# Kernel optimization log

Measured on AMD Instinct MI355X. Metric: run time of the kernel, lower is better.

Reference implementation:

```python
import jax, jax.numpy as jnp
import numpy as np

N_NODES = 50000
N_EDGES = 1600000
F_IN = 256
HID = 256
HEADS = 8
HD = HID // HEADS  # 32
SLOPE = 0.2
EPS = 1e-5


def setup_inputs() -> dict:
    key = jax.random.key(0)
    ks = jax.random.split(key, 10)
    node_features = jax.random.normal(ks[0], (N_NODES, F_IN), jnp.float32)
    edge_index = jax.random.randint(ks[1], (2, N_EDGES), 0, N_NODES, jnp.int32)
    s = 1.0 / np.sqrt(F_IN)
    W = jax.random.uniform(ks[2], (HEADS, F_IN, HD), jnp.float32, -s, s)
    bw = jax.random.uniform(ks[3], (HEADS, HD), jnp.float32, -s, s)
    sa = 1.0 / np.sqrt(2 * HD)
    A = jax.random.uniform(ks[4], (HEADS, 2 * HD), jnp.float32, -sa, sa)
    ba = jax.random.uniform(ks[5], (HEADS,), jnp.float32, -sa, sa)
    gamma = jnp.ones((HEADS, HD), jnp.float32)
    beta = jnp.zeros((HEADS, HD), jnp.float32)
    so = 1.0 / np.sqrt(HD)
    Wout = jax.random.uniform(ks[6], (HD, HID), jnp.float32, -so, so)
    bout = jax.random.uniform(ks[7], (HID,), jnp.float32, -so, so)
    return dict(node_features=node_features, edge_index=edge_index, W=W, bw=bw,
                A=A, ba=ba, gamma=gamma, beta=beta, Wout=Wout, bout=bout)


def _head(x, W, bw, a, ba, gamma, beta, tgt, src):
    h = x @ W + bw                         # [N, d]
    # attn(concat(h_i, h_j)) = h_i @ a1 + h_j @ a2 + ba  (linear over concat)
    si = h @ a[:HD]                        # [N]
    sj = h @ a[HD:]                        # [N]
    e = si[tgt] + sj[src] + ba             # [E]
    e = jnp.where(e >= 0, e, SLOPE * e)    # leaky_relu
    # scatter_softmax over edges grouped by target node (stable)
    m = jax.ops.segment_max(e, tgt, num_segments=N_NODES)
    ex = jnp.exp(e - m[tgt])
    den = jax.ops.segment_sum(ex, tgt, num_segments=N_NODES)
    alpha = ex / den[tgt]                  # [E]  (dropout in eval mode = identity)
    msg = alpha[:, None] * h[src]          # [E, d]
    agg = jax.ops.segment_sum(msg, tgt, num_segments=N_NODES)  # [N, d]
    out = agg + h                          # skip connection
    out = jnp.where(out > 0, out, jnp.expm1(out))  # ELU
    mu = out.mean(axis=-1, keepdims=True)
    var = out.var(axis=-1, keepdims=True)
    return (out - mu) * jax.lax.rsqrt(var + EPS) * gamma + beta


def reference(node_features, edge_index, W, bw, A, ba, gamma, beta, Wout, bout):
    tgt = edge_index[0]
    src = edge_index[1]
    heads = jax.vmap(_head, in_axes=(None, 0, 0, 0, 0, 0, 0, None, None))(
        node_features, W, bw, A, ba, gamma, beta, tgt, src)   # [H, N, d]
    mean = heads.mean(axis=0)                                  # [N, d]
    y = mean @ Wout + bout                                     # [N, HID]
    return jnp.where(y > 0, y, jnp.expm1(y))                   # ELU
```

## Files before the change

kernel.cpp:

```cpp
#include <hip/hip_runtime.h>
#include <hip/hip_bf16.h>
#include <hip/hip_fp16.h>

#define N_NODES 50000
#define N_EDGES 1600000
#define HEADS 8
#define HD 32
#define FIN 256
#define HID 256

typedef unsigned short u16;
typedef unsigned int u32;

typedef short s8v __attribute__((ext_vector_type(8)));
typedef float f4v __attribute__((ext_vector_type(4)));
typedef float fx4 __attribute__((ext_vector_type(4)));

__device__ __forceinline__ u32 pk2(float lo, float hi) {
  __hip_bfloat162 b = __float22bfloat162_rn(make_float2(lo, hi));
  union { __hip_bfloat162 b2; u32 u; } c;
  c.b2 = b;
  return c.u;
}

__global__ __launch_bounds__(256) void k_prepw(const float* __restrict__ W,
                                               u16* __restrict__ Wp) {
  int id = blockIdx.x * 256 + threadIdx.x;
  int col = id >> 8;
  int k = id & 255;
  int h = col >> 5, d = col & 31;
  Wp[col * 256 + k] = (u16)(pk2(W[h * 8192 + k * 32 + d], 0.f) & 0xFFFFu);
}

#define GEMM_BLOCKS ((N_NODES + 127) / 128)
__global__ __launch_bounds__(512) void k_gemhist(
    const float* __restrict__ X, const u16* __restrict__ Wp,
    const float* __restrict__ bw, const float* __restrict__ A,
    __half* __restrict__ Hb, float* __restrict__ si, float* __restrict__ sj,
    const int* __restrict__ tgt, int* __restrict__ cnt, int* __restrict__ rank) {
  __shared__ __align__(16) u16 Xs[128 * 40];
  __shared__ __align__(16) u16 Wt[256 * 40];

  if (blockIdx.x >= GEMM_BLOCKS) {
    int e = (blockIdx.x - GEMM_BLOCKS) * 512 + threadIdx.x;
    if (e < N_EDGES) {
      int tg = __builtin_nontemporal_load(tgt + e);
      rank[e] = atomicAdd(&cnt[tg], 1);
    }
    return;
  }

  const int t = threadIdx.x;
  const int m0 = blockIdx.x * 128;
  const int w = t >> 6;
  const int lane = t & 63;
  const int l15 = lane & 15;
  const int quad = lane >> 4;
  const int wm = (w >> 2) * 64;
  const int wn = (w & 3) * 64;

  f4v acc[4][4];
#pragma unroll
  for (int i = 0; i < 4; i++)
#pragma unroll
    for (int j = 0; j < 4; j++) acc[i][j] = (f4v){0.f, 0.f, 0.f, 0.f};

  const int wcol = t >> 2;
  const int wpart = t & 3;

  for (int k0 = 0; k0 < FIN; k0 += 32) {
#pragma unroll
    for (int p = 0; p < 2; p++) {
      int row = p * 64 + (t >> 3);
      int f4 = t & 7;
      int node = m0 + row;
      fx4 xv = (fx4){0.f, 0.f, 0.f, 0.f};
      if (node < N_NODES)
        xv = __builtin_nontemporal_load((const fx4*)&X[node * FIN + k0 + f4 * 4]);
      u32* dst = (u32*)&Xs[row * 40 + f4 * 4];
      dst[0] = pk2(xv[0], xv[1]);
      dst[1] = pk2(xv[2], xv[3]);
    }
#pragma unroll
    for (int c2 = 0; c2 < 2; c2++) {
      int cc = wcol + c2 * 128;
      *(fx4*)&Wt[cc * 40 + wpart * 8] =
          *(const fx4*)&Wp[cc * 256 + k0 + wpart * 8];
    }
    __syncthreads();
    s8v af[4], bf[4];
#pragma unroll
    for (int mi = 0; mi < 4; mi++)
      af[mi] = *(const s8v*)&Xs[(wm + mi * 16 + l15) * 40 + quad * 8];
#pragma unroll
    for (int ni = 0; ni < 4; ni++)
      bf[ni] = *(const s8v*)&Wt[(wn + ni * 16 + l15) * 40 + quad * 8];
#pragma unroll
    for (int mi = 0; mi < 4; mi++)
#pragma unroll
      for (int ni = 0; ni < 4; ni++)
        acc[mi][ni] = __builtin_amdgcn_mfma_f32_16x16x32_bf16(af[mi], bf[ni], acc[mi][ni], 0, 0, 0);
    __syncthreads();
  }

  const int head0 = wn >> 5;
  const int head1 = head0 + 1;
  float c1a0 = A[head0 * 64 + l15],      c1a1 = A[head0 * 64 + 16 + l15];
  float c2a0 = A[head0 * 64 + 32 + l15], c2a1 = A[head0 * 64 + 48 + l15];
  float c1b0 = A[head1 * 64 + l15],      c1b1 = A[head1 * 64 + 16 + l15];
  float c2b0 = A[head1 * 64 + 32 + l15], c2b1 = A[head1 * 64 + 48 + l15];

#pragma unroll
  for (int mi = 0; mi < 4; mi++) {
#pragma unroll
    for (int ni = 0; ni < 4; ni++) {
      float b = bw[wn + ni * 16 + l15];
#pragma unroll
      for (int r = 0; r < 4; r++) acc[mi][ni][r] += b;
    }
    const int rbase = m0 + wm + mi * 16 + quad * 4;
#pragma unroll
    for (int r = 0; r < 4; r++) {
      int node = rbase + r;
      if (node < N_NODES) {
#pragma unroll
        for (int ni = 0; ni < 4; ni++) {
          int col = wn + ni * 16 + l15;
          Hb[node * HID + col] = __float2half_rn(acc[mi][ni][r]);
        }
      }
    }
    float s1a[4], s2a[4], s1b[4], s2b[4];
#pragma unroll
    for (int r = 0; r < 4; r++) {
      s1a[r] = acc[mi][0][r] * c1a0 + acc[mi][1][r] * c1a1;
      s2a[r] = acc[mi][0][r] * c2a0 + acc[mi][1][r] * c2a1;
      s1b[r] = acc[mi][2][r] * c1b0 + acc[mi][3][r] * c1b1;
      s2b[r] = acc[mi][2][r] * c2b0 + acc[mi][3][r] * c2b1;
    }
#pragma unroll
    for (int off = 1; off <= 8; off <<= 1) {
#pragma unroll
      for (int r = 0; r < 4; r++) {
        s1a[r] += __shfl_xor(s1a[r], off);
        s2a[r] += __shfl_xor(s2a[r], off);
        s1b[r] += __shfl_xor(s1b[r], off);
        s2b[r] += __shfl_xor(s2b[r], off);
      }
    }
    if (l15 == 0) {
#pragma unroll
      for (int r = 0; r < 4; r++) {
        int node = rbase + r;
        if (node < N_NODES) {
          si[node * HEADS + head0] = s1a[r];
          sj[node * HEADS + head0] = s2a[r];
          si[node * HEADS + head1] = s1b[r];
          sj[node * HEADS + head1] = s2b[r];
        }
      }
    }
  }
}

#define SCHUNK 49
__global__ __launch_bounds__(1024) void k_scan(const int* __restrict__ cnt,
                                               int* __restrict__ rowptr) {
  __shared__ int s[1024];
  const int t = threadIdx.x;
  const int base = t * SCHUNK;
  int sum = 0;
#pragma unroll 7
  for (int j = 0; j < SCHUNK; j++) {
    int i = base + j;
    sum += (i < N_NODES) ? cnt[i] : 0;
  }
  s[t] = sum;
  __syncthreads();
  int x = sum;
  for (int off = 1; off < 1024; off <<= 1) {
    int y = (t >= off) ? s[t - off] : 0;
    __syncthreads();
    x += y;
    s[t] = x;
    __syncthreads();
  }
  int run = x - sum;
#pragma unroll 7
  for (int j = 0; j < SCHUNK; j++) {
    int i = base + j;
    if (i < N_NODES) {
      rowptr[i] = run;
      run += cnt[i];
    }
  }
}

__global__ void k_scatter(const int* __restrict__ tgt, const int* __restrict__ src,
                          const int* __restrict__ rowptr, const int* __restrict__ rank,
                          int* __restrict__ sortedSrc) {
  int e = blockIdx.x * 256 + threadIdx.x;
  if (e < N_EDGES) {
    int tg = __builtin_nontemporal_load(tgt + e);
    int sc = __builtin_nontemporal_load(src + e);
    int rk = __builtin_nontemporal_load(rank + e);
    sortedSrc[rowptr[tg] + rk] = sc;
  }
}

__global__ __launch_bounds__(256) void k_fused(
    const __half* __restrict__ Hb, const float* __restrict__ si,
    const float* __restrict__ sj, const float* __restrict__ ba,
    const float* __restrict__ gamma, const float* __restrict__ beta,
    const float* __restrict__ Wout, const float* __restrict__ bout,
    const int* __restrict__ rowptr, const int* __restrict__ cnt,
    const int* __restrict__ sortedSrc, float* __restrict__ out) {
  const int t = threadIdx.x;
  const int lane = t & 63;
  const int n = blockIdx.x * 4 + (t >> 6);
  const int cg = lane & 31;
  const int es = lane >> 5;
  const int hh = cg >> 2;
  const int start = rowptr[n];
  const int deg = cnt[n];

  const float sb = si[n * HEADS + hh] + ba[hh];
  const char* hbBase = (const char*)Hb + 16 * cg;
  const int* ss = sortedSrc + start;

  float acc[8] = {0.f, 0.f, 0.f, 0.f, 0.f, 0.f, 0.f, 0.f};
  float den = 0.f;
#pragma unroll 4
  for (int slot = es; slot < deg; slot += 2) {
    int s = __builtin_nontemporal_load(ss + slot);
    float e = sb + sj[s * HEADS + hh];
    e = (e >= 0.f) ? e : 0.2f * e;
    float exv = __expf(e);
    float4 hb4 = *(const float4*)(hbBase + (size_t)s * (HID * 2));
    const __half2* hp = (const __half2*)&hb4;
#pragma unroll
    for (int d = 0; d < 4; d++) {
      acc[2 * d]     += exv * __low2float(hp[d]);
      acc[2 * d + 1] += exv * __high2float(hp[d]);
    }
    den += exv;
  }
#pragma unroll
  for (int j = 0; j < 8; j++) acc[j] += __shfl_xor(acc[j], 32);
  den += __shfl_xor(den, 32);

  float4 h4 = *(const float4*)((const char*)Hb + (size_t)n * (HID * 2) + 16 * cg);
  const __half2* hq = (const __half2*)&h4;
  float inv = (deg > 0) ? __fdividef(1.f, den) : 0.f;
  float v[8], sum = 0.f, sq = 0.f;
#pragma unroll
  for (int j = 0; j < 8; j++) {
    float hv = (j & 1) ? __high2float(hq[j >> 1]) : __low2float(hq[j >> 1]);
    float x = acc[j] * inv + hv;
    x = (x > 0.f) ? x : (__expf(x) - 1.f);
    v[j] = x;
    sum += x;
    sq += x * x;
  }
  sum += __shfl_xor(sum, 1); sq += __shfl_xor(sq, 1);
  sum += __shfl_xor(sum, 2); sq += __shfl_xor(sq, 2);
  float mu = sum * (1.f / 32.f);
  float var = sq * (1.f / 32.f) - mu * mu;
  float rstd = rsqrtf(var + 1e-5f);
  fx4 g0 = *(const fx4*)&gamma[cg * 8];
  fx4 g1 = *(const fx4*)&gamma[cg * 8 + 4];
  fx4 b0 = *(const fx4*)&beta[cg * 8];
  fx4 b1 = *(const fx4*)&beta[cg * 8 + 4];
  float m2[8];
#pragma unroll
  for (int j = 0; j < 8; j++) {
    float g = (j < 4) ? g0[j] : g1[j - 4];
    float bb = (j < 4) ? b0[j] : b1[j - 4];
    m2[j] = (v[j] - mu) * rstd * g + bb;
  }
#pragma unroll
  for (int j = 0; j < 8; j++) {
    m2[j] += __shfl_xor(m2[j], 4);
    m2[j] += __shfl_xor(m2[j], 8);
    m2[j] += __shfl_xor(m2[j], 16);
  }
  fx4 y = *(const fx4*)&bout[4 * lane];
#pragma unroll
  for (int q = 0; q < 4; q++) {
    float mv[8];
#pragma unroll
    for (int j = 0; j < 8; j++) mv[j] = __shfl(m2[j], q) * 0.125f;
#pragma unroll
    for (int j = 0; j < 8; j++) {
      fx4 w4 = *(const fx4*)&Wout[(q * 8 + j) * HID + 4 * lane];
      y += mv[j] * w4;
    }
  }
#pragma unroll
  for (int c = 0; c < 4; c++) y[c] = (y[c] > 0.f) ? y[c] : (__expf(y[c]) - 1.f);
  __builtin_nontemporal_store(y, (fx4*)&out[(size_t)n * HID + 4 * lane]);
}

extern "C" void kernel_launch(void* const* d_in, const int* in_sizes, int n_in,
                              void* d_out, int out_size, void* d_ws, size_t ws_size,
                              hipStream_t stream) {
  const float* X     = (const float*)d_in[0];
  const int*   EI    = (const int*)d_in[1];
  const float* W     = (const float*)d_in[2];
  const float* bw    = (const float*)d_in[3];
  const float* A     = (const float*)d_in[4];
  const float* ba    = (const float*)d_in[5];
  const float* gamma = (const float*)d_in[6];
  const float* beta  = (const float*)d_in[7];
  const float* Wout  = (const float*)d_in[8];
  const float* bout  = (const float*)d_in[9];
  float* out = (float*)d_out;
  const int* tgt = EI;
  const int* src = EI + N_EDGES;

  char* ws = (char*)d_ws;
  size_t off = 0;
  auto alloc = [&](size_t bytes) -> void* {
    void* p = ws + off;
    off += bytes;
    off = (off + 255) & ~(size_t)255;
    return p;
  };
  __half* Hb       = (__half*)alloc((size_t)N_NODES * HID * 2);
  float* si        = (float*)alloc((size_t)N_NODES * HEADS * 4);
  float* sj        = (float*)alloc((size_t)N_NODES * HEADS * 4);
  int*   cnt       = (int*)  alloc((size_t)N_NODES * 4);
  int*   rowptr    = (int*)  alloc((size_t)N_NODES * 4);
  int*   rank      = (int*)  alloc((size_t)N_EDGES * 4);
  int*   sortedSrc = (int*)  alloc((size_t)N_EDGES * 4);
  u16*   Wp        = (u16*)  alloc((size_t)HID * FIN * 2);

  hipMemsetAsync(cnt, 0, (size_t)N_NODES * 4, stream);
  k_prepw<<<256, 256, 0, stream>>>(W, Wp);
  k_gemhist<<<GEMM_BLOCKS + (N_EDGES + 511) / 512, 512, 0, stream>>>(
      X, Wp, bw, A, Hb, si, sj, tgt, cnt, rank);
  k_scan<<<1, 1024, 0, stream>>>(cnt, rowptr);
  k_scatter<<<(N_EDGES + 255) / 256, 256, 0, stream>>>(tgt, src, rowptr, rank, sortedSrc);
  k_fused<<<(N_NODES + 3) / 4, 256, 0, stream>>>(Hb, si, sj, ba, gamma, beta,
                                                 Wout, bout, rowptr, cnt,
                                                 sortedSrc, out);
}
```

Baseline: 471.0 us.

## Split GEMM tiles across histogram and scatter phases to overlap work

The GEMM tiles are moved into a device function and split into two groups. The first group runs alongside the edge histogram in one kernel, and the rest run alongside the edge scatter in a second kernel, replacing the separate scatter launch. The aim is to balance compute-heavy GEMM work against memory- and atomic-bound edge work in both phases and to hide the single-block scan's idle time. The scatter blocks change from 256 to 512 threads and now carry GEMM's LDS allocation, which may reduce occupancy.

```diff
diff --git a/kernel.cpp b/kernel.cpp
--- a/kernel.cpp
+++ b/kernel.cpp
@@ -32,26 +32,13 @@
   Wp[col * 256 + k] = (u16)(pk2(W[h * 8192 + k * 32 + d], 0.f) & 0xFFFFu);
 }
 
-#define GEMM_BLOCKS ((N_NODES + 127) / 128)
-__global__ __launch_bounds__(512) void k_gemhist(
-    const float* __restrict__ X, const u16* __restrict__ Wp,
+__device__ __forceinline__ void gemm_tile(
+    int gb, const float* __restrict__ X, const u16* __restrict__ Wp,
     const float* __restrict__ bw, const float* __restrict__ A,
     __half* __restrict__ Hb, float* __restrict__ si, float* __restrict__ sj,
-    const int* __restrict__ tgt, int* __restrict__ cnt, int* __restrict__ rank) {
-  __shared__ __align__(16) u16 Xs[128 * 40];
-  __shared__ __align__(16) u16 Wt[256 * 40];
-
-  if (blockIdx.x >= GEMM_BLOCKS) {
-    int e = (blockIdx.x - GEMM_BLOCKS) * 512 + threadIdx.x;
-    if (e < N_EDGES) {
-      int tg = __builtin_nontemporal_load(tgt + e);
-      rank[e] = atomicAdd(&cnt[tg], 1);
-    }
-    return;
-  }
-
+    u16* Xs, u16* Wt) {
   const int t = threadIdx.x;
-  const int m0 = blockIdx.x * 128;
+  const int m0 = gb * 128;
   const int w = t >> 6;
   const int lane = t & 63;
   const int l15 = lane & 15;
@@ -159,6 +146,29 @@
           sj[node * HEADS + head1] = s2b[r];
         }
       }
+    }
+  }
+}
+
+#define GEMM_BLOCKS ((N_NODES + 127) / 128)
+#define GA 192
+#define GB (GEMM_BLOCKS - GA)
+#define EB512 ((N_EDGES + 511) / 512)
+
+__global__ __launch_bounds__(512) void k_ph1(
+    const float* __restrict__ X, const u16* __restrict__ Wp,
+    const float* __restrict__ bw, const float* __restrict__ A,
+    __half* __restrict__ Hb, float* __restrict__ si, float* __restrict__ sj,
+    const int* __restrict__ tgt, int* __restrict__ cnt, int* __restrict__ rank) {
+  __shared__ __align__(16) u16 Xs[128 * 40];
+  __shared__ __align__(16) u16 Wt[256 * 40];
+  if (blockIdx.x < GA) {
+    gemm_tile(blockIdx.x, X, Wp, bw, A, Hb, si, sj, Xs, Wt);
+  } else {
+    int e = (blockIdx.x - GA) * 512 + threadIdx.x;
+    if (e < N_EDGES) {
+      int tg = __builtin_nontemporal_load(tgt + e);
+      rank[e] = atomicAdd(&cnt[tg], 1);
     }
   }
 }
@@ -196,15 +206,25 @@
   }
 }
 
-__global__ void k_scatter(const int* __restrict__ tgt, const int* __restrict__ src,
-                          const int* __restrict__ rowptr, const int* __restrict__ rank,
-                          int* __restrict__ sortedSrc) {
-  int e = blockIdx.x * 256 + threadIdx.x;
-  if (e < N_EDGES) {
-    int tg = __builtin_nontemporal_load(tgt + e);
-    int sc = __builtin_nontemporal_load(src + e);
-    int rk = __builtin_nontemporal_load(rank + e);
-    sortedSrc[rowptr[tg] + rk] = sc;
+__global__ __launch_bounds__(512) void k_ph2(
+    const float* __restrict__ X, const u16* __restrict__ Wp,
+    const float* __restrict__ bw, const float* __restrict__ A,
+    __half* __restrict__ Hb, float* __restrict__ si, float* __restrict__ sj,
+    const int* __restrict__ tgt, const int* __restrict__ src,
+    const int* __restrict__ rowptr, const int* __restrict__ rank,
+    int* __restrict__ sortedSrc) {
+  __shared__ __align__(16) u16 Xs[128 * 40];
+  __shared__ __align__(16) u16 Wt[256 * 40];
+  if (blockIdx.x < GB) {
+    gemm_tile(GA + blockIdx.x, X, Wp, bw, A, Hb, si, sj, Xs, Wt);
+  } else {
+    int e = (blockIdx.x - GB) * 512 + threadIdx.x;
+    if (e < N_EDGES) {
+      int tg = __builtin_nontemporal_load(tgt + e);
+      int sc = __builtin_nontemporal_load(src + e);
+      int rk = __builtin_nontemporal_load(rank + e);
+      sortedSrc[rowptr[tg] + rk] = sc;
+    }
   }
 }
 
@@ -337,10 +357,10 @@
 
   hipMemsetAsync(cnt, 0, (size_t)N_NODES * 4, stream);
   k_prepw<<<256, 256, 0, stream>>>(W, Wp);
-  k_gemhist<<<GEMM_BLOCKS + (N_EDGES + 511) / 512, 512, 0, stream>>>(
-      X, Wp, bw, A, Hb, si, sj, tgt, cnt, rank);
+  k_ph1<<<GA + EB512, 512, 0, stream>>>(X, Wp, bw, A, Hb, si, sj, tgt, cnt, rank);
   k_scan<<<1, 1024, 0, stream>>>(cnt, rowptr);
-  k_scatter<<<(N_EDGES + 255) / 256, 256, 0, stream>>>(tgt, src, rowptr, rank, sortedSrc);
+  k_ph2<<<GB + EB512, 512, 0, stream>>>(X, Wp, bw, A, Hb, si, sj, tgt, src,
+                                        rowptr, rank, sortedSrc);
   k_fused<<<(N_NODES + 3) / 4, 256, 0, stream>>>(Hb, si, sj, ba, gamma, beta,
                                                  Wout, bout, rowptr, cnt,
                                                  sortedSrc, out);
```

New measurement: 488.3 us. 3.7% more time.
